# Performance work log

Hardware: AMD Instinct MI355X
Metric: run time of the kernel (lower is better)

The kernel has to match this reference:

```python
import jax, jax.numpy as jnp
import numpy as np

N = 30000
DEG = 16
E_RAND = N * DEG
E = E_RAND + N  # with self loops appended
T = 2
F_IN, H1, OUT = 128, 128, 64
NBSZ = 15
AGG = 0.8
NEG_SLOPE = 0.2


def setup_inputs() -> dict:
    key = jax.random.key(0)
    ks = jax.random.split(key, 10)
    x_all = jax.random.normal(ks[0], (T, N, F_IN), dtype=jnp.float32)
    # edges per snapshot: random edges + self loops (mirrors remove_self_loops + add_self_loops)
    loops = jnp.arange(N, dtype=jnp.int32)
    eis = []
    for t in range(T):
        src = jax.random.randint(jax.random.fold_in(ks[1], t), (E_RAND,), 0, N, dtype=jnp.int32)
        dst = jax.random.randint(jax.random.fold_in(ks[2], t), (E_RAND,), 0, N, dtype=jnp.int32)
        eis.append(jnp.stack([jnp.concatenate([src, loops]), jnp.concatenate([dst, loops])]))
    edge_index_all = jnp.stack(eis)  # [T, 2, E]
    def glorot(k, shape):
        fan = shape[0] + shape[-1]
        s = jnp.sqrt(6.0 / fan)
        return jax.random.uniform(k, shape, jnp.float32, -s, s)
    W1 = glorot(ks[3], (F_IN, 2 * H1))
    att1 = glorot(ks[4], (1, 1, 4 * H1))   # [1, heads=1, 2*out_neurons]
    b1 = jnp.zeros((2 * H1,), jnp.float32)
    W2 = glorot(ks[5], (H1, 2 * OUT))
    att2 = glorot(ks[6], (1, 1, 4 * OUT))
    b2 = jnp.zeros((2 * OUT,), jnp.float32)
    return {"x_all": x_all, "edge_index_all": edge_index_all,
            "W1": W1, "att1": att1, "b1": b1, "W2": W2, "att2": att2, "b2": b2}


def _conv(x, edge_index, W, att, b, C):
    """One DGIBConv (heads=1, Bernoulli distribution, diag reparam, eval mode).
    Returns (node_out [N,C], ixz scalar, structure_kl scalar)."""
    h = x @ W                                    # [N, 2C]
    src, dst = edge_index[0], edge_index[1]
    x_j = h[src]                                 # [E, 2C] per-edge gather (source)
    x_i = h[dst]                                 # [E, 2C] target
    a = att[0, 0]                                # [4C]
    logits = jnp.sum(x_i * a[:2 * C], -1) + jnp.sum(x_j * a[2 * C:], -1)  # [E]
    logits = jax.nn.leaky_relu(logits, NEG_SLOPE)
    # Bernoulli branch: softmax of ones over segments == 1/deg(dst)
    deg = jax.ops.segment_sum(jnp.ones_like(logits), dst, num_segments=N)  # [N]
    norm = 1.0 / deg[dst]
    p = jnp.clip(jax.nn.sigmoid(logits), 0.01, 0.99)  # posterior Bernoulli probs
    alpha = p * norm
    aggr = jax.ops.segment_sum(x_j * alpha[:, None], dst, num_segments=N) + b  # [N, 2C]
    # diag reparam: mean || std-logit split; Gaussian prior N(0, I)
    mu = aggr[:, :C]
    std = jax.nn.softplus(aggr[:, C:]) + 1e-10
    kl = -jnp.log(std) + 0.5 * (std * std + mu * mu) - 0.5  # KL(N(mu,std)||N(0,1)) per dim
    ixz = jnp.mean(jnp.sum(kl, -1))
    # structure KL: Bernoulli(p) || Bernoulli(logits = 1/nbsz)
    q = jax.nn.sigmoid(jnp.float32(1.0 / NBSZ))
    skl = jnp.mean(p * jnp.log(p / q) + (1.0 - p) * jnp.log((1.0 - p) / (1.0 - q)))
    return mu, ixz, skl


def _layer(x_list, edge_index_all, W, att, b, C):
    """Temporal DGIBConv.forward: per-snapshot conv + weighted temporal fusion."""
    outs, ixzs, skls = [], [], []
    for t in range(T):
        out, ixz, skl = _conv(x_list[t], edge_index_all[t], W, att, b, C)
        if t > 0:
            w = jax.nn.sigmoid(jnp.arange(t, dtype=jnp.float32))[:, None, None]  # [t,1,1]
            prev = jnp.stack(outs[:t])                                           # [t,N,C]
            out = jnp.sum(w * prev, 0) / t * AGG + out * (1.0 - AGG)
        outs.append(out)
        ixzs.append(ixz)
        skls.append(skl)
    return outs, jnp.mean(jnp.stack(ixzs)), jnp.mean(jnp.stack(skls))


def reference(x_all, edge_index_all, W1, att1, b1, W2, att2, b2):
    xs = [x_all[t] for t in range(T)]
    h1, ixz1, skl1 = _layer(xs, edge_index_all, W1, att1, b1, H1)
    h1 = [jax.nn.relu(h) for h in h1]  # with_relu=True, eval -> dropout is identity
    h2, ixz2, skl2 = _layer(h1, edge_index_all, W2, att2, b2, OUT)
    out = jnp.stack(h2)                # [T, N, OUT]
    ixz_mean = (ixz1 + ixz2) / 2.0
    skl_mean = (skl1 + skl2) / 2.0
    return out, ixz_mean, skl_mean
```

## Files before the change

kernel.cpp:

```cpp
#include <hip/hip_runtime.h>
#include <hip/hip_bf16.h>

#define N_NODES 30000
#define N_EDGES 510000
#define K_DIM   128
#define ABLK    7500
#define EBLK    997

typedef short bf16x8 __attribute__((ext_vector_type(8)));
typedef float f32x4  __attribute__((ext_vector_type(4)));
typedef float f32x2  __attribute__((ext_vector_type(2)));
typedef unsigned int u32x2 __attribute__((ext_vector_type(2)));

__device__ __forceinline__ unsigned short f2bf(float f) {
  __hip_bfloat16 h = __float2bfloat16(f);
  return *(unsigned short*)&h;
}

__global__ void transpose_w_kernel(const float* __restrict__ W1, unsigned short* __restrict__ Wt1,
                                   const float* __restrict__ W2, unsigned short* __restrict__ Wt2) {
  int i = blockIdx.x * blockDim.x + threadIdx.x;
  if (i < 128 * 256) {
    int k = i >> 8, m = i & 255;
    Wt1[m * 128 + k] = f2bf(W1[i]);
  } else if (i < 128 * 256 + 128 * 128) {
    int j = i - 128 * 256;
    int k = j >> 7, m = j & 127;
    Wt2[m * 128 + k] = f2bf(W2[j]);
  }
}

__global__ void deg_kernel(const int* __restrict__ ei, int* __restrict__ deg0,
                           int* __restrict__ deg1, int e) {
  int i = blockIdx.x * blockDim.x + threadIdx.x;
  if (i < 2 * e) {
    int t = i >= e ? 1 : 0;
    int j = i - t * e;
    int d = ei[(size_t)t * 2 * e + e + j];
    atomicAdd(&(t ? deg1 : deg0)[d], 1);
  }
}

__global__ __launch_bounds__(1024) void scan_kernel(const int* __restrict__ deg0, int* __restrict__ off0,
                                                    int* __restrict__ cur0, float* __restrict__ rn0,
                                                    const int* __restrict__ deg1, int* __restrict__ off1,
                                                    int* __restrict__ cur1, float* __restrict__ rn1,
                                                    int n) {
  const int* deg = blockIdx.x ? deg1 : deg0;
  int* off = blockIdx.x ? off1 : off0;
  int* cur = blockIdx.x ? cur1 : cur0;
  float* rn = blockIdx.x ? rn1 : rn0;
  const int CHUNK = 30;
  __shared__ int wsum[16];
  int tid = threadIdx.x;
  int base = tid * CHUNK;
  int sum = 0;
  for (int i = 0; i < CHUNK; i++)
    if (base + i < n) sum += deg[base + i];
  int lane = tid & 63, wid = tid >> 6;
  int incl = sum;
#pragma unroll
  for (int o = 1; o < 64; o <<= 1) {
    int v = __shfl_up(incl, o);
    if (lane >= o) incl += v;
  }
  if (lane == 63) wsum[wid] = incl;
  __syncthreads();
  if (tid == 0) {
    int run = 0;
    for (int w = 0; w < 16; w++) { int v = wsum[w]; wsum[w] = run; run += v; }
  }
  __syncthreads();
  int run = incl - sum + wsum[wid];
  for (int i = 0; i < CHUNK; i++) {
    if (base + i < n) {
      int dg = deg[base + i];
      off[base + i] = run;
      cur[base + i] = run;
      rn[base + i] = 1.0f / (float)dg;
      run += dg;
    }
  }
}

__global__ void scatter_kernel(const int* __restrict__ ei,
                               int* __restrict__ cur0, int* __restrict__ cur1,
                               unsigned int* __restrict__ csr0, unsigned int* __restrict__ csr1, int e) {
  int i = blockIdx.x * blockDim.x + threadIdx.x;
  if (i < 2 * e) {
    int t = i >= e ? 1 : 0;
    int j = i - t * e;
    int s = ei[(size_t)t * 2 * e + j];
    int d = ei[(size_t)t * 2 * e + e + j];
    int* cur = t ? cur1 : cur0;
    unsigned int* csr = t ? csr1 : csr0;
    int p = atomicAdd(&cur[d], 1);
    csr[p] = (unsigned int)s | ((unsigned int)d << 16);
  }
}

template<int M, int MODE>
__global__ __launch_bounds__(256) void gemm_kernel(const void* __restrict__ X0v,
                                                   const void* __restrict__ X1v,
                                                   const short* __restrict__ Wt,
                                                   unsigned char* __restrict__ H0,
                                                   unsigned char* __restrict__ H1,
                                                   const float* __restrict__ att,
                                                   float* __restrict__ si0, float* __restrict__ si1,
                                                   float* __restrict__ sj0, float* __restrict__ sj1,
                                                   int nrows) {
  int t = blockIdx.y;
  unsigned char* Hf8 = t ? H1 : H0;
  float* s_i = t ? si1 : si0;
  float* s_j = t ? sj1 : sj0;

  int wave = blockIdx.x * 4 + (threadIdx.x >> 6);
  int lane = threadIdx.x & 63;
  if (wave * 16 >= nrows) return;
  int m16 = lane & 15, quad = lane >> 4;

  bf16x8 a[4];
  size_t arow = (size_t)(wave * 16 + m16) * K_DIM + quad * 8;
  if constexpr (MODE == 0) {
    const float* X = (const float*)(t ? X1v : X0v);
#pragma unroll
    for (int kc = 0; kc < 4; kc++) {
      f32x4 lo = *(const f32x4*)(X + arow + kc * 32);
      f32x4 hi = *(const f32x4*)(X + arow + kc * 32 + 4);
#pragma unroll
      for (int j = 0; j < 4; j++) {
        ((unsigned short*)&a[kc])[j]     = f2bf(lo[j]);
        ((unsigned short*)&a[kc])[4 + j] = f2bf(hi[j]);
      }
    }
  } else {
    const float* Xa = (const float*)X0v;
    const float* Xb = (const float*)X1v;
#pragma unroll
    for (int kc = 0; kc < 4; kc++) {
      f32x4 lo = *(const f32x4*)(Xa + arow + kc * 32);
      f32x4 hi = *(const f32x4*)(Xa + arow + kc * 32 + 4);
      if (t) {
        f32x4 lo1 = *(const f32x4*)(Xb + arow + kc * 32);
        f32x4 hi1 = *(const f32x4*)(Xb + arow + kc * 32 + 4);
        lo = lo * 0.4f + lo1 * 0.2f;
        hi = hi * 0.4f + hi1 * 0.2f;
      }
#pragma unroll
      for (int j = 0; j < 4; j++) {
        ((unsigned short*)&a[kc])[j]     = f2bf(fmaxf(lo[j], 0.f));
        ((unsigned short*)&a[kc])[4 + j] = f2bf(fmaxf(hi[j], 0.f));
      }
    }
  }

  float sip[4] = {0.f, 0.f, 0.f, 0.f}, sjp[4] = {0.f, 0.f, 0.f, 0.f};
#pragma unroll
  for (int nt = 0; nt < M / 16; nt++) {
    f32x4 acc = {0.f, 0.f, 0.f, 0.f};
    size_t brow = (size_t)(nt * 16 + m16) * K_DIM + quad * 8;
#pragma unroll
    for (int kc = 0; kc < 4; kc++) {
      bf16x8 b = *(const bf16x8*)(Wt + brow + kc * 32);
      acc = __builtin_amdgcn_mfma_f32_16x16x32_bf16(a[kc], b, acc, 0, 0, 0);
    }
    int col = nt * 16 + m16;
    float aA = att[col], aB = att[M + col];
#pragma unroll
    for (int r = 0; r < 4; r++) {
      int row = wave * 16 + quad * 4 + r;
      int pk = __builtin_amdgcn_cvt_pk_fp8_f32(acc[r], acc[r], 0, false);
      Hf8[(size_t)row * M + col] = (unsigned char)pk;
      sip[r] += acc[r] * aA;
      sjp[r] += acc[r] * aB;
    }
  }
#pragma unroll
  for (int o = 1; o < 16; o <<= 1) {
#pragma unroll
    for (int r = 0; r < 4; r++) {
      sip[r] += __shfl_xor(sip[r], o);
      sjp[r] += __shfl_xor(sjp[r], o);
    }
  }
  if (m16 == 0) {
#pragma unroll
    for (int r = 0; r < 4; r++) {
      int row = wave * 16 + quad * 4 + r;
      s_i[row] = sip[r];
      s_j[row] = sjp[r];
    }
  }
}

__global__ __launch_bounds__(256) void edge_kernel(const unsigned int* __restrict__ csr_0,
                                                   const unsigned int* __restrict__ csr_1,
                                                   const float* __restrict__ rn0, const float* __restrict__ rn1,
                                                   const float* __restrict__ si0, const float* __restrict__ si1,
                                                   const float* __restrict__ sj0, const float* __restrict__ sj1,
                                                   unsigned int* __restrict__ iw0, unsigned int* __restrict__ iw1,
                                                   float* __restrict__ epart,
                                                   int e) {
  int t = blockIdx.y;
  const unsigned int* csr = t ? csr_1 : csr_0;
  const float* rn = t ? rn1 : rn0;
  const float* s_i = t ? si1 : si0;
  const float* s_j = t ? sj1 : sj0;
  unsigned int* iw = t ? iw1 : iw0;

  const float q   = 1.0f / (1.0f + __expf(-(1.0f / 15.0f)));
  const float lq  = __logf(q);
  const float l1q = __logf(1.0f - q);

  __shared__ float red[4];
  float skl = 0.f;
  int p0 = (blockIdx.x * 256 + threadIdx.x) * 2;
#pragma unroll
  for (int u = 0; u < 2; u++) {
    int p = p0 + u;
    if (p < e) {
      unsigned int sd = csr[p];
      int s = (int)(sd & 0xffffu);
      int dd = (int)(sd >> 16);
      float lg = s_i[dd] + s_j[s];
      lg = lg > 0.f ? lg : 0.2f * lg;
      float pv = 1.0f / (1.0f + __expf(-lg));
      pv = fminf(fmaxf(pv, 0.01f), 0.99f);
      skl += pv * (__logf(pv) - lq) + (1.0f - pv) * (__logf(1.0f - pv) - l1q);
      float w = pv * rn[dd];
      iw[p] = (unsigned int)s | ((unsigned int)f2bf(w) << 16);
    }
  }
  int lane = threadIdx.x & 63, wid = threadIdx.x >> 6;
#pragma unroll
  for (int o = 32; o > 0; o >>= 1) skl += __shfl_xor(skl, o);
  if (lane == 0) red[wid] = skl;
  __syncthreads();
  if (threadIdx.x == 0) epart[t * EBLK + blockIdx.x] = red[0] + red[1] + red[2] + red[3];
}

template<int M>
__global__ __launch_bounds__(256) void aggr_kernel(const unsigned char* __restrict__ H0,
                                                   const unsigned char* __restrict__ H1,
                                                   const unsigned int* __restrict__ iw0,
                                                   const unsigned int* __restrict__ iw1,
                                                   const int* __restrict__ off0, const int* __restrict__ off1,
                                                   const int* __restrict__ deg0, const int* __restrict__ deg1,
                                                   const float* __restrict__ bias,
                                                   float* __restrict__ mu0, float* __restrict__ mu1,
                                                   float* __restrict__ apart,
                                                   int n) {
  constexpr int C = M / 2;
  constexpr int HB = M / 2;
  constexpr int LPR = HB / 8;
  constexpr int L2LPR = (M == 256) ? 4 : 3;
  constexpr int EPL = 64 / LPR;
  constexpr int NL = 4;
  constexpr int U = NL * EPL;

  int y = blockIdx.y;
  int t = y >> 1, q = y & 1;
  const unsigned char* Hf8 = t ? H1 : H0;
  const unsigned int* iw = t ? iw1 : iw0;
  const int* off = t ? off1 : off0;
  const int* deg = t ? deg1 : deg0;
  float* mu = t ? mu1 : mu0;

  __shared__ float red_i[4];
  int wid = threadIdx.x >> 6, lane = threadIdx.x & 63;
  int wave = blockIdx.x * 4 + wid;
  float ixz = 0.f;

  if (wave < n) {
    int d     = __builtin_amdgcn_readfirstlane(deg[wave]);
    int start = __builtin_amdgcn_readfirstlane(off[wave]);
    const unsigned int* iwp = iw + start;
    int sub = lane & (LPR - 1);
    int g   = lane >> L2LPR;
    const unsigned char* hbase = Hf8 + q * HB + sub * 8;

    f32x2 acc[4];
#pragma unroll
    for (int k = 0; k < 4; k++) acc[k] = {0.f, 0.f};

    for (int e0 = 0; e0 < d; e0 += U) {
      unsigned int iwl[NL];
#pragma unroll
      for (int l = 0; l < NL; l++) {
        int e = e0 + l * EPL + g;
        iwl[l] = iwp[e < d ? e : d - 1];
      }
      u32x2 hv[NL];
#pragma unroll
      for (int l = 0; l < NL; l++)
        hv[l] = *(const u32x2*)(hbase + (size_t)(iwl[l] & 0xffffu) * M);
#pragma unroll
      for (int l = 0; l < NL; l++) {
        int e = e0 + l * EPL + g;
        float wf = (e < d) ? __uint_as_float(iwl[l] & 0xffff0000u) : 0.f;
        f32x2 wv = {wf, wf};
        f32x2 d0 = __builtin_amdgcn_cvt_pk_f32_fp8((int)hv[l][0], false);
        f32x2 d1 = __builtin_amdgcn_cvt_pk_f32_fp8((int)hv[l][0], true);
        f32x2 d2 = __builtin_amdgcn_cvt_pk_f32_fp8((int)hv[l][1], false);
        f32x2 d3 = __builtin_amdgcn_cvt_pk_f32_fp8((int)hv[l][1], true);
        acc[0] = d0 * wv + acc[0];
        acc[1] = d1 * wv + acc[1];
        acc[2] = d2 * wv + acc[2];
        acc[3] = d3 * wv + acc[3];
      }
    }

#pragma unroll
    for (int o = LPR; o < 64; o <<= 1) {
#pragma unroll
      for (int j = 0; j < 4; j++) {
        acc[j][0] += __shfl_xor(acc[j][0], o);
        acc[j][1] += __shfl_xor(acc[j][1], o);
      }
    }

    if (lane < LPR) {
      int ch0 = q * HB + sub * 8;
      if (q == 0) {
        f32x4 mv[2];
#pragma unroll
        for (int j = 0; j < 4; j++) {
          float a0 = acc[j][0] + bias[ch0 + 2 * j];
          float a1 = acc[j][1] + bias[ch0 + 2 * j + 1];
          ixz += 0.5f * (a0 * a0 + a1 * a1) - 1.0f;
          mv[j >> 1][(j & 1) * 2]     = a0;
          mv[j >> 1][(j & 1) * 2 + 1] = a1;
        }
        *(f32x4*)(mu + (size_t)wave * C + ch0)     = mv[0];
        *(f32x4*)(mu + (size_t)wave * C + ch0 + 4) = mv[1];
      } else {
#pragma unroll
        for (int j = 0; j < 4; j++) {
#pragma unroll
          for (int h = 0; h < 2; h++) {
            float a = acc[j][h] + bias[ch0 + 2 * j + h];
            float sp = (a > 20.f) ? a : log1pf(__expf(a));
            sp += 1e-10f;
            ixz += -__logf(sp) + 0.5f * sp * sp;
          }
        }
      }
    }
  }
#pragma unroll
  for (int o = 32; o > 0; o >>= 1) ixz += __shfl_xor(ixz, o);
  if (lane == 0) red_i[wid] = ixz;
  __syncthreads();
  if (threadIdx.x == 0)
    apart[y * ABLK + blockIdx.x] = red_i[0] + red_i[1] + red_i[2] + red_i[3];
}

__global__ void fuse2_kernel(const float* __restrict__ mu0, const float* __restrict__ mu1,
                             float* __restrict__ out, int n) {
  int i = blockIdx.x * blockDim.x + threadIdx.x;
  if (i < n) {
    float m0 = mu0[i], m1 = mu1[i];
    out[i] = m0;
    out[n + i] = 0.4f * m0 + 0.2f * m1;
  }
}

__global__ __launch_bounds__(1024) void reduce_kernel(const float* __restrict__ a1,
                                                      const float* __restrict__ a2,
                                                      const float* __restrict__ e1,
                                                      const float* __restrict__ e2,
                                                      float* __restrict__ out2) {
  __shared__ float ri[16], rs[16];
  float ixz = 0.f, skl = 0.f;
  for (int i = threadIdx.x; i < 4 * ABLK; i += 1024) ixz += a1[i] + a2[i];
  for (int i = threadIdx.x; i < 2 * EBLK; i += 1024) skl += e1[i] + e2[i];
  int lane = threadIdx.x & 63, wid = threadIdx.x >> 6;
#pragma unroll
  for (int o = 32; o > 0; o >>= 1) {
    ixz += __shfl_xor(ixz, o);
    skl += __shfl_xor(skl, o);
  }
  if (lane == 0) { ri[wid] = ixz; rs[wid] = skl; }
  __syncthreads();
  if (threadIdx.x == 0) {
    float si = 0.f, ss = 0.f;
    for (int w = 0; w < 16; w++) { si += ri[w]; ss += rs[w]; }
    out2[0] = si / (4.0f * (float)N_NODES);
    out2[1] = ss / (4.0f * (float)N_EDGES);
  }
}

extern "C" void kernel_launch(void* const* d_in, const int* in_sizes, int n_in,
                              void* d_out, int out_size, void* d_ws, size_t ws_size,
                              hipStream_t stream) {
  const float* x_all = (const float*)d_in[0];
  const int* ei      = (const int*)d_in[1];
  const float* W1    = (const float*)d_in[2];
  const float* att1  = (const float*)d_in[3];
  const float* b1    = (const float*)d_in[4];
  const float* W2    = (const float*)d_in[5];
  const float* att2  = (const float*)d_in[6];
  const float* b2    = (const float*)d_in[7];
  float* out         = (float*)d_out;

  char* ws = (char*)d_ws;
  size_t off = 0;
  auto alloc = [&](size_t bytes) {
    char* p = ws + off;
    off = (off + bytes + 255) & ~(size_t)255;
    return p;
  };
  unsigned short* wt1  = (unsigned short*)alloc(256 * 128 * sizeof(short));
  unsigned short* wt2  = (unsigned short*)alloc(128 * 128 * sizeof(short));
  unsigned char* hf8_0 = (unsigned char*)alloc((size_t)N_NODES * 256);
  unsigned char* hf8_1 = (unsigned char*)alloc((size_t)N_NODES * 256);
  float* si0   = (float*)alloc(N_NODES * sizeof(float));
  float* si1   = (float*)alloc(N_NODES * sizeof(float));
  float* sj0   = (float*)alloc(N_NODES * sizeof(float));
  float* sj1   = (float*)alloc(N_NODES * sizeof(float));
  float* mu1_0 = (float*)alloc((size_t)N_NODES * 128 * sizeof(float));
  float* mu1_1 = (float*)alloc((size_t)N_NODES * 128 * sizeof(float));
  float* mu2_0 = mu1_0;
  float* mu2_1 = mu1_0 + (size_t)N_NODES * 64;
  unsigned int* iwp[2] = {(unsigned int*)alloc((size_t)N_EDGES * 4),
                          (unsigned int*)alloc((size_t)N_EDGES * 4)};
  int* degp[2]  = {(int*)alloc(N_NODES * 4), (int*)alloc(N_NODES * 4)};
  int* offp[2]  = {(int*)alloc(N_NODES * 4), (int*)alloc(N_NODES * 4)};
  int* curp[2]  = {(int*)alloc(N_NODES * 4), (int*)alloc(N_NODES * 4)};
  float* rnp[2] = {(float*)alloc(N_NODES * 4), (float*)alloc(N_NODES * 4)};
  unsigned int* csrp[2] = {(unsigned int*)alloc((size_t)N_EDGES * 4),
                           (unsigned int*)alloc((size_t)N_EDGES * 4)};
  float* apart1 = (float*)alloc(4 * ABLK * sizeof(float));
  float* apart2 = (float*)alloc(4 * ABLK * sizeof(float));
  float* epart1 = (float*)alloc(2 * EBLK * sizeof(float));
  float* epart2 = (float*)alloc(2 * EBLK * sizeof(float));

  hipMemsetAsync(degp[0], 0, N_NODES * 4, stream);
  hipMemsetAsync(degp[1], 0, N_NODES * 4, stream);

  transpose_w_kernel<<<192, 256, 0, stream>>>(W1, wt1, W2, wt2);

  deg_kernel<<<(2 * N_EDGES + 255) / 256, 256, 0, stream>>>(ei, degp[0], degp[1], N_EDGES);
  scan_kernel<<<2, 1024, 0, stream>>>(degp[0], offp[0], curp[0], rnp[0],
                                      degp[1], offp[1], curp[1], rnp[1], N_NODES);
  scatter_kernel<<<(2 * N_EDGES + 255) / 256, 256, 0, stream>>>(ei, curp[0], curp[1],
                                                                csrp[0], csrp[1], N_EDGES);

  dim3 ggrid(469, 2), egrid(EBLK, 2), agrid(ABLK, 4);

  const float* x0 = x_all;
  const float* x1 = x_all + (size_t)N_NODES * K_DIM;
  gemm_kernel<256, 0><<<ggrid, 256, 0, stream>>>(x0, x1, (const short*)wt1, hf8_0, hf8_1,
                                                 att1, si0, si1, sj0, sj1, N_NODES);
  edge_kernel<<<egrid, 256, 0, stream>>>(csrp[0], csrp[1], rnp[0], rnp[1],
                                         si0, si1, sj0, sj1, iwp[0], iwp[1], epart1, N_EDGES);
  aggr_kernel<256><<<agrid, 256, 0, stream>>>(hf8_0, hf8_1, iwp[0], iwp[1], offp[0], offp[1],
                                              degp[0], degp[1], b1, mu1_0, mu1_1, apart1, N_NODES);

  gemm_kernel<128, 1><<<ggrid, 256, 0, stream>>>(mu1_0, mu1_1, (const short*)wt2, hf8_0, hf8_1,
                                                 att2, si0, si1, sj0, sj1, N_NODES);
  edge_kernel<<<egrid, 256, 0, stream>>>(csrp[0], csrp[1], rnp[0], rnp[1],
                                         si0, si1, sj0, sj1, iwp[0], iwp[1], epart2, N_EDGES);
  aggr_kernel<128><<<agrid, 256, 0, stream>>>(hf8_0, hf8_1, iwp[0], iwp[1], offp[0], offp[1],
                                              degp[0], degp[1], b2, mu2_0, mu2_1, apart2, N_NODES);
  fuse2_kernel<<<(N_NODES * 64 + 255) / 256, 256, 0, stream>>>(mu2_0, mu2_1, out, N_NODES * 64);
  reduce_kernel<<<1, 1024, 0, stream>>>(apart1, apart2, epart1, epart2, out + (size_t)2 * N_NODES * 64);
}
```

Measured before the change: 636.5 us.

## Fuse edge logit computation into CSR aggregation kernel and merge prep kernels

Removes the separate edge kernel. Each aggregation wave now computes the edge logits, the Bernoulli probabilities and the structure KL for its destination row, then broadcasts source indices and weights through wave shuffles. The aggregation also stops splitting each row into two channel halves across grid.y, so one wave covers the whole row. The weight transpose and degree count are merged into one prep kernel, and the two degree memsets become one. This drops the intermediate per-edge weight array and several launches, at the cost of more work per wave and fewer waves in the aggregation grid.

Result: faster. 603.2 us (-5.2%).

```diff
diff --git a/kernel.cpp b/kernel.cpp
--- a/kernel.cpp
+++ b/kernel.cpp
@@ -5,7 +5,6 @@
 #define N_EDGES 510000
 #define K_DIM   128
 #define ABLK    7500
-#define EBLK    997
 
 typedef short bf16x8 __attribute__((ext_vector_type(8)));
 typedef float f32x4  __attribute__((ext_vector_type(4)));
@@ -17,8 +16,10 @@
   return *(unsigned short*)&h;
 }
 
-__global__ void transpose_w_kernel(const float* __restrict__ W1, unsigned short* __restrict__ Wt1,
-                                   const float* __restrict__ W2, unsigned short* __restrict__ Wt2) {
+__global__ void prep_kernel(const float* __restrict__ W1, unsigned short* __restrict__ Wt1,
+                            const float* __restrict__ W2, unsigned short* __restrict__ Wt2,
+                            const int* __restrict__ ei, int* __restrict__ deg0,
+                            int* __restrict__ deg1, int e) {
   int i = blockIdx.x * blockDim.x + threadIdx.x;
   if (i < 128 * 256) {
     int k = i >> 8, m = i & 255;
@@ -28,11 +29,6 @@
     int k = j >> 7, m = j & 127;
     Wt2[m * 128 + k] = f2bf(W2[j]);
   }
-}
-
-__global__ void deg_kernel(const int* __restrict__ ei, int* __restrict__ deg0,
-                           int* __restrict__ deg1, int e) {
-  int i = blockIdx.x * blockDim.x + threadIdx.x;
   if (i < 2 * e) {
     int t = i >= e ? 1 : 0;
     int j = i - t * e;
@@ -193,120 +189,98 @@
   }
 }
 
-__global__ __launch_bounds__(256) void edge_kernel(const unsigned int* __restrict__ csr_0,
-                                                   const unsigned int* __restrict__ csr_1,
+template<int M>
+__global__ __launch_bounds__(256) void aggr_kernel(const unsigned char* __restrict__ H0,
+                                                   const unsigned char* __restrict__ H1,
+                                                   const unsigned int* __restrict__ csr0,
+                                                   const unsigned int* __restrict__ csr1,
+                                                   const int* __restrict__ off0, const int* __restrict__ off1,
+                                                   const int* __restrict__ deg0, const int* __restrict__ deg1,
                                                    const float* __restrict__ rn0, const float* __restrict__ rn1,
                                                    const float* __restrict__ si0, const float* __restrict__ si1,
                                                    const float* __restrict__ sj0, const float* __restrict__ sj1,
-                                                   unsigned int* __restrict__ iw0, unsigned int* __restrict__ iw1,
-                                                   float* __restrict__ epart,
-                                                   int e) {
+                                                   const float* __restrict__ bias,
+                                                   float* __restrict__ mu0, float* __restrict__ mu1,
+                                                   f32x2* __restrict__ part,
+                                                   int n) {
+  constexpr int C = M / 2;
+  constexpr int LPR = M / 8;
+  constexpr int L2LPR = (M == 256) ? 5 : 4;
+  constexpr int EPL = 64 / LPR;
+  constexpr int NL = 4;
+  constexpr int U = NL * EPL;
+
   int t = blockIdx.y;
-  const unsigned int* csr = t ? csr_1 : csr_0;
+  const unsigned char* Hf8 = t ? H1 : H0;
+  const unsigned int* csr = t ? csr1 : csr0;
+  const int* off = t ? off1 : off0;
+  const int* deg = t ? deg1 : deg0;
   const float* rn = t ? rn1 : rn0;
   const float* s_i = t ? si1 : si0;
   const float* s_j = t ? sj1 : sj0;
-  unsigned int* iw = t ? iw1 : iw0;
-
-  const float q   = 1.0f / (1.0f + __expf(-(1.0f / 15.0f)));
-  const float lq  = __logf(q);
-  const float l1q = __logf(1.0f - q);
-
-  __shared__ float red[4];
-  float skl = 0.f;
-  int p0 = (blockIdx.x * 256 + threadIdx.x) * 2;
-#pragma unroll
-  for (int u = 0; u < 2; u++) {
-    int p = p0 + u;
-    if (p < e) {
-      unsigned int sd = csr[p];
-      int s = (int)(sd & 0xffffu);
-      int dd = (int)(sd >> 16);
-      float lg = s_i[dd] + s_j[s];
+  float* mu = t ? mu1 : mu0;
+
+  __shared__ f32x2 red[4];
+  int wid = threadIdx.x >> 6, lane = threadIdx.x & 63;
+  int wave = blockIdx.x * 4 + wid;
+  float ixz = 0.f, skl = 0.f;
+
+  if (wave < n) {
+    int d     = __builtin_amdgcn_readfirstlane(deg[wave]);
+    int start = __builtin_amdgcn_readfirstlane(off[wave]);
+    float siv = s_i[wave];
+    float rnv = rn[wave];
+    int sub = lane & (LPR - 1);
+    int g   = lane >> L2LPR;
+    const unsigned char* hbase = Hf8 + sub * 8;
+
+    const float qc  = 1.0f / (1.0f + __expf(-(1.0f / 15.0f)));
+    const float lq  = __logf(qc);
+    const float l1q = __logf(1.0f - qc);
+
+    f32x2 acc[4];
+#pragma unroll
+    for (int k = 0; k < 4; k++) acc[k] = {0.f, 0.f};
+
+    for (int base = 0; base < d; base += 64) {
+      int ee = base + lane;
+      unsigned int ce = csr[start + (ee < d ? ee : d - 1)];
+      int src = (int)(ce & 0xffffu);
+      float sj = s_j[src];
+      float lg = siv + sj;
       lg = lg > 0.f ? lg : 0.2f * lg;
       float pv = 1.0f / (1.0f + __expf(-lg));
       pv = fminf(fmaxf(pv, 0.01f), 0.99f);
-      skl += pv * (__logf(pv) - lq) + (1.0f - pv) * (__logf(1.0f - pv) - l1q);
-      float w = pv * rn[dd];
-      iw[p] = (unsigned int)s | ((unsigned int)f2bf(w) << 16);
-    }
-  }
-  int lane = threadIdx.x & 63, wid = threadIdx.x >> 6;
-#pragma unroll
-  for (int o = 32; o > 0; o >>= 1) skl += __shfl_xor(skl, o);
-  if (lane == 0) red[wid] = skl;
-  __syncthreads();
-  if (threadIdx.x == 0) epart[t * EBLK + blockIdx.x] = red[0] + red[1] + red[2] + red[3];
-}
-
-template<int M>
-__global__ __launch_bounds__(256) void aggr_kernel(const unsigned char* __restrict__ H0,
-                                                   const unsigned char* __restrict__ H1,
-                                                   const unsigned int* __restrict__ iw0,
-                                                   const unsigned int* __restrict__ iw1,
-                                                   const int* __restrict__ off0, const int* __restrict__ off1,
-                                                   const int* __restrict__ deg0, const int* __restrict__ deg1,
-                                                   const float* __restrict__ bias,
-                                                   float* __restrict__ mu0, float* __restrict__ mu1,
-                                                   float* __restrict__ apart,
-                                                   int n) {
-  constexpr int C = M / 2;
-  constexpr int HB = M / 2;
-  constexpr int LPR = HB / 8;
-  constexpr int L2LPR = (M == 256) ? 4 : 3;
-  constexpr int EPL = 64 / LPR;
-  constexpr int NL = 4;
-  constexpr int U = NL * EPL;
-
-  int y = blockIdx.y;
-  int t = y >> 1, q = y & 1;
-  const unsigned char* Hf8 = t ? H1 : H0;
-  const unsigned int* iw = t ? iw1 : iw0;
-  const int* off = t ? off1 : off0;
-  const int* deg = t ? deg1 : deg0;
-  float* mu = t ? mu1 : mu0;
-
-  __shared__ float red_i[4];
-  int wid = threadIdx.x >> 6, lane = threadIdx.x & 63;
-  int wave = blockIdx.x * 4 + wid;
-  float ixz = 0.f;
-
-  if (wave < n) {
-    int d     = __builtin_amdgcn_readfirstlane(deg[wave]);
-    int start = __builtin_amdgcn_readfirstlane(off[wave]);
-    const unsigned int* iwp = iw + start;
-    int sub = lane & (LPR - 1);
-    int g   = lane >> L2LPR;
-    const unsigned char* hbase = Hf8 + q * HB + sub * 8;
-
-    f32x2 acc[4];
-#pragma unroll
-    for (int k = 0; k < 4; k++) acc[k] = {0.f, 0.f};
-
-    for (int e0 = 0; e0 < d; e0 += U) {
-      unsigned int iwl[NL];
-#pragma unroll
-      for (int l = 0; l < NL; l++) {
-        int e = e0 + l * EPL + g;
-        iwl[l] = iwp[e < d ? e : d - 1];
-      }
-      u32x2 hv[NL];
-#pragma unroll
-      for (int l = 0; l < NL; l++)
-        hv[l] = *(const u32x2*)(hbase + (size_t)(iwl[l] & 0xffffu) * M);
-#pragma unroll
-      for (int l = 0; l < NL; l++) {
-        int e = e0 + l * EPL + g;
-        float wf = (e < d) ? __uint_as_float(iwl[l] & 0xffff0000u) : 0.f;
-        f32x2 wv = {wf, wf};
-        f32x2 d0 = __builtin_amdgcn_cvt_pk_f32_fp8((int)hv[l][0], false);
-        f32x2 d1 = __builtin_amdgcn_cvt_pk_f32_fp8((int)hv[l][0], true);
-        f32x2 d2 = __builtin_amdgcn_cvt_pk_f32_fp8((int)hv[l][1], false);
-        f32x2 d3 = __builtin_amdgcn_cvt_pk_f32_fp8((int)hv[l][1], true);
-        acc[0] = d0 * wv + acc[0];
-        acc[1] = d1 * wv + acc[1];
-        acc[2] = d2 * wv + acc[2];
-        acc[3] = d3 * wv + acc[3];
+      if (ee < d)
+        skl += pv * (__logf(pv) - lq) + (1.0f - pv) * (__logf(1.0f - pv) - l1q);
+      float wval = (ee < d) ? pv * rnv : 0.f;
+
+      int cnt = min(d - base, 64);
+      for (int c0 = 0; c0 < cnt; c0 += U) {
+        int srcl[NL];
+        float wl[NL];
+#pragma unroll
+        for (int l = 0; l < NL; l++) {
+          int idx = c0 + l * EPL + g;
+          srcl[l] = __shfl(src, idx);
+          wl[l]   = __shfl(wval, idx);
+        }
+        u32x2 hv[NL];
+#pragma unroll
+        for (int l = 0; l < NL; l++)
+          hv[l] = *(const u32x2*)(hbase + (size_t)srcl[l] * M);
+#pragma unroll
+        for (int l = 0; l < NL; l++) {
+          f32x2 wv = {wl[l], wl[l]};
+          f32x2 d0 = __builtin_amdgcn_cvt_pk_f32_fp8((int)hv[l][0], false);
+          f32x2 d1 = __builtin_amdgcn_cvt_pk_f32_fp8((int)hv[l][0], true);
+          f32x2 d2 = __builtin_amdgcn_cvt_pk_f32_fp8((int)hv[l][1], false);
+          f32x2 d3 = __builtin_amdgcn_cvt_pk_f32_fp8((int)hv[l][1], true);
+          acc[0] = d0 * wv + acc[0];
+          acc[1] = d1 * wv + acc[1];
+          acc[2] = d2 * wv + acc[2];
+          acc[3] = d3 * wv + acc[3];
+        }
       }
     }
 
@@ -320,8 +294,8 @@
     }
 
     if (lane < LPR) {
-      int ch0 = q * HB + sub * 8;
-      if (q == 0) {
+      int ch0 = sub * 8;
+      if (ch0 < C) {
         f32x4 mv[2];
 #pragma unroll
         for (int j = 0; j < 4; j++) {
@@ -348,11 +322,16 @@
     }
   }
 #pragma unroll
-  for (int o = 32; o > 0; o >>= 1) ixz += __shfl_xor(ixz, o);
-  if (lane == 0) red_i[wid] = ixz;
+  for (int o = 32; o > 0; o >>= 1) {
+    ixz += __shfl_xor(ixz, o);
+    skl += __shfl_xor(skl, o);
+  }
+  if (lane == 0) { f32x2 r; r[0] = ixz; r[1] = skl; red[wid] = r; }
   __syncthreads();
-  if (threadIdx.x == 0)
-    apart[y * ABLK + blockIdx.x] = red_i[0] + red_i[1] + red_i[2] + red_i[3];
+  if (threadIdx.x == 0) {
+    f32x2 pr = red[0] + red[1] + red[2] + red[3];
+    part[t * ABLK + blockIdx.x] = pr;
+  }
 }
 
 __global__ void fuse2_kernel(const float* __restrict__ mu0, const float* __restrict__ mu1,
@@ -365,15 +344,16 @@
   }
 }
 
-__global__ __launch_bounds__(1024) void reduce_kernel(const float* __restrict__ a1,
-                                                      const float* __restrict__ a2,
-                                                      const float* __restrict__ e1,
-                                                      const float* __restrict__ e2,
+__global__ __launch_bounds__(1024) void reduce_kernel(const f32x2* __restrict__ p1,
+                                                      const f32x2* __restrict__ p2,
                                                       float* __restrict__ out2) {
   __shared__ float ri[16], rs[16];
   float ixz = 0.f, skl = 0.f;
-  for (int i = threadIdx.x; i < 4 * ABLK; i += 1024) ixz += a1[i] + a2[i];
-  for (int i = threadIdx.x; i < 2 * EBLK; i += 1024) skl += e1[i] + e2[i];
+  for (int i = threadIdx.x; i < 2 * ABLK; i += 1024) {
+    f32x2 a = p1[i], b = p2[i];
+    ixz += a[0] + b[0];
+    skl += a[1] + b[1];
+  }
   int lane = threadIdx.x & 63, wid = threadIdx.x >> 6;
 #pragma unroll
   for (int o = 32; o > 0; o >>= 1) {
@@ -422,47 +402,40 @@
   float* mu1_1 = (float*)alloc((size_t)N_NODES * 128 * sizeof(float));
   float* mu2_0 = mu1_0;
   float* mu2_1 = mu1_0 + (size_t)N_NODES * 64;
-  unsigned int* iwp[2] = {(unsigned int*)alloc((size_t)N_EDGES * 4),
-                          (unsigned int*)alloc((size_t)N_EDGES * 4)};
-  int* degp[2]  = {(int*)alloc(N_NODES * 4), (int*)alloc(N_NODES * 4)};
+  int* degbase  = (int*)alloc(2 * N_NODES * 4);
+  int* degp[2]  = {degbase, degbase + N_NODES};
   int* offp[2]  = {(int*)alloc(N_NODES * 4), (int*)alloc(N_NODES * 4)};
   int* curp[2]  = {(int*)alloc(N_NODES * 4), (int*)alloc(N_NODES * 4)};
   float* rnp[2] = {(float*)alloc(N_NODES * 4), (float*)alloc(N_NODES * 4)};
   unsigned int* csrp[2] = {(unsigned int*)alloc((size_t)N_EDGES * 4),
                            (unsigned int*)alloc((size_t)N_EDGES * 4)};
-  float* apart1 = (float*)alloc(4 * ABLK * sizeof(float));
-  float* apart2 = (float*)alloc(4 * ABLK * sizeof(float));
-  float* epart1 = (float*)alloc(2 * EBLK * sizeof(float));
-  float* epart2 = (float*)alloc(2 * EBLK * sizeof(float));
-
-  hipMemsetAsync(degp[0], 0, N_NODES * 4, stream);
-  hipMemsetAsync(degp[1], 0, N_NODES * 4, stream);
-
-  transpose_w_kernel<<<192, 256, 0, stream>>>(W1, wt1, W2, wt2);
-
-  deg_kernel<<<(2 * N_EDGES + 255) / 256, 256, 0, stream>>>(ei, degp[0], degp[1], N_EDGES);
+  f32x2* part1 = (f32x2*)alloc(2 * ABLK * sizeof(f32x2));
+  f32x2* part2 = (f32x2*)alloc(2 * ABLK * sizeof(f32x2));
+
+  hipMemsetAsync(degbase, 0, 2 * N_NODES * 4, stream);
+
+  prep_kernel<<<(2 * N_EDGES + 255) / 256, 256, 0, stream>>>(W1, wt1, W2, wt2,
+                                                             ei, degp[0], degp[1], N_EDGES);
   scan_kernel<<<2, 1024, 0, stream>>>(degp[0], offp[0], curp[0], rnp[0],
                                       degp[1], offp[1], curp[1], rnp[1], N_NODES);
   scatter_kernel<<<(2 * N_EDGES + 255) / 256, 256, 0, stream>>>(ei, curp[0], curp[1],
                                                                 csrp[0], csrp[1], N_EDGES);
 
-  dim3 ggrid(469, 2), egrid(EBLK, 2), agrid(ABLK, 4);
+  dim3 ggrid(469, 2), agrid(ABLK, 2);
 
   const float* x0 = x_all;
   const float* x1 = x_all + (size_t)N_NODES * K_DIM;
   gemm_kernel<256, 0><<<ggrid, 256, 0, stream>>>(x0, x1, (const short*)wt1, hf8_0, hf8_1,
                                                  att1, si0, si1, sj0, sj1, N_NODES);
-  edge_kernel<<<egrid, 256, 0, stream>>>(csrp[0], csrp[1], rnp[0], rnp[1],
-                                         si0, si1, sj0, sj1, iwp[0], iwp[1], epart1, N_EDGES);
-  aggr_kernel<256><<<agrid, 256, 0, stream>>>(hf8_0, hf8_1, iwp[0], iwp[1], offp[0], offp[1],
-                                              degp[0], degp[1], b1, mu1_0, mu1_1, apart1, N_NODES);
+  aggr_kernel<256><<<agrid, 256, 0, stream>>>(hf8_0, hf8_1, csrp[0], csrp[1], offp[0], offp[1],
+                                              degp[0], degp[1], rnp[0], rnp[1],
+                                              si0, si1, sj0, sj1, b1, mu1_0, mu1_1, part1, N_NODES);
 
   gemm_kernel<128, 1><<<ggrid, 256, 0, stream>>>(mu1_0, mu1_1, (const short*)wt2, hf8_0, hf8_1,
                                                  att2, si0, si1, sj0, sj1, N_NODES);
-  edge_kernel<<<egrid, 256, 0, stream>>>(csrp[0], csrp[1], rnp[0], rnp[1],
-                                         si0, si1, sj0, sj1, iwp[0], iwp[1], epart2, N_EDGES);
-  aggr_kernel<128><<<agrid, 256, 0, stream>>>(hf8_0, hf8_1, iwp[0], iwp[1], offp[0], offp[1],
-                                              degp[0], degp[1], b2, mu2_0, mu2_1, apart2, N_NODES);
+  aggr_kernel<128><<<agrid, 256, 0, stream>>>(hf8_0, hf8_1, csrp[0], csrp[1], offp[0], offp[1],
+                                              degp[0], degp[1], rnp[0], rnp[1],
+                                              si0, si1, sj0, sj1, b2, mu2_0, mu2_1, part2, N_NODES);
   fuse2_kernel<<<(N_NODES * 64 + 255) / 256, 256, 0, stream>>>(mu2_0, mu2_1, out, N_NODES * 64);
-  reduce_kernel<<<1, 1024, 0, stream>>>(apart1, apart2, epart1, epart2, out + (size_t)2 * N_NODES * 64);
-}
+  reduce_kernel<<<1, 1024, 0, stream>>>(part1, part2, out + (size_t)2 * N_NODES * 64);
+}
```
